# Kernel optimization log

Hardware: AMD Instinct MI355X
Metric: run time of the kernel (lower is better)

Reference implementation:

```python
import math
import jax
import jax.numpy as jnp
import numpy as np

B, N = 64, 64
R = N * (N - 1)
DIST_THRESH = 0.35


def _pair_indices(n):
    # edge e = i*(n-1) + j - (j > i): row-major over i, ascending j skipping j == i
    ii = np.repeat(np.arange(n), n - 1)
    jm = np.tile(np.arange(n), (n, 1))
    jj = jm[~np.eye(n, dtype=bool)].reshape(-1)
    return ii, jj


def _rot_basis(a):
    # a: [..., 1] angle -> [..., 2, 2] rotation basis rows [cos,sin],[cos(a+pi/2),sin(a+pi/2)]
    first = jnp.concatenate([jnp.cos(a), jnp.sin(a)], axis=-1)
    second = jnp.concatenate([jnp.cos(a + math.pi / 2), jnp.sin(a + math.pi / 2)], axis=-1)
    return jnp.stack([first, second], axis=-2)


def setup_inputs() -> dict:
    ks = jax.random.split(jax.random.key(0), 8)
    nrm = lambda k, shape, s=1.0: (jax.random.normal(k, shape) * s).astype(jnp.float32)
    return dict(
        objects_state=jax.random.uniform(ks[0], (B, N, 8), dtype=jnp.float32),
        objects_shape=nrm(ks[1], (B, N, 10)),
        relation_info=nrm(ks[2], (B, R, 3)),
        s_mean=jnp.zeros((8,), jnp.float32), s_std=jnp.ones((8,), jnp.float32),
        sh_mean=jnp.zeros((10,), jnp.float32), sh_std=jnp.ones((10,), jnp.float32),
        v_mean=jnp.zeros((3,), jnp.float32), v_std=jnp.ones((3,), jnp.float32),
        W1=nrm(ks[3], (32, 256), 32 ** -0.5), b1=jnp.zeros((256,), jnp.float32),
        W2=nrm(ks[4], (256, 128), 256 ** -0.5), b2=jnp.zeros((128,), jnp.float32),
        W3=nrm(ks[5], (141, 256), 141 ** -0.5), b3=jnp.zeros((256,), jnp.float32),
        W4=nrm(ks[6], (256, 3), 256 ** -0.5), b4=jnp.zeros((3,), jnp.float32),
    )


def reference(objects_state, objects_shape, relation_info, s_mean, s_std, sh_mean, sh_std,
              v_mean, v_std, W1, b1, W2, b2, W3, b3, W4, b4):
    n = objects_state.shape[1]
    ii, jj = _pair_indices(n)

    # ---- pre_proces: distance-threshold edge build into dense one-hot matrices ----
    pos = objects_state[:, :, 0:2]
    dist = jnp.sqrt(jnp.sum((pos[:, :, None, :] - pos[:, None, :, :]) ** 2, axis=-1))
    # torch: where(dist<0.35, dist, 0).nonzero() -> keeps dist<0.35 AND dist != 0 (drops self-edges)
    mask = ((dist < DIST_THRESH) & (dist != 0.0)).astype(jnp.float32)
    mask_flat = mask[:, ii, jj]  # [B, R]
    eye = jnp.eye(n, dtype=jnp.float32)
    receiver_relations = mask_flat[:, :, None] * eye[ii][None]  # [B, R, N]
    sender_relations = mask_flat[:, :, None] * eye[jj][None]    # [B, R, N]

    data_state = (objects_state - s_mean) / s_std
    data_shape = (objects_shape - sh_mean) / sh_std

    senders_state = jnp.einsum('brn,bnd->brd', sender_relations, data_state)
    receivers_state = jnp.einsum('brn,bnd->brd', receiver_relations, data_state)
    senders_shape = jnp.einsum('brn,bnd->brd', sender_relations, data_shape)
    receivers_shape = jnp.einsum('brn,bnd->brd', receiver_relations, data_shape)

    basis = _rot_basis(receivers_state[:, :, 2:3])  # [B, R, 2, 2]
    diff_state = senders_state - receivers_state
    temp = jnp.stack([diff_state[:, :, 0:2], diff_state[:, :, 3:5], senders_state[:, :, 6:8]], axis=-1)  # [B,R,2,3]
    tfed = jnp.einsum('brij,brjk->brik', basis, temp)  # [B,R,2,3]
    angle_diff = diff_state[:, :, 2:3]
    diff_feat = jnp.concatenate([
        tfed[:, :, :, 0], tfed[:, :, :, 1], tfed[:, :, :, 2],
        jnp.sin(2 * angle_diff), jnp.cos(2 * angle_diff),
        diff_state[:, :, 5:6],
    ], axis=-1)  # [B, R, 9]
    rel_data = jnp.concatenate([relation_info, diff_feat, receivers_shape, senders_shape], axis=-1)  # [B,R,32]

    obj_basis = _rot_basis(data_state[:, :, 2:3])  # [B, N, 2, 2]
    obj_vel_tfed = jnp.einsum('bnij,bnj->bni', obj_basis, data_state[:, :, 3:5])
    obj_data = jnp.concatenate([obj_vel_tfed, data_state[:, :, 5:6], data_shape], axis=-1)  # [B,N,13]

    # ---- interaction-network Net ----
    effects = jax.nn.relu(rel_data @ W1 + b1) @ W2 + b2  # [B, R, 128]
    agg = jnp.einsum('brn,bre->bne', receiver_relations, effects)  # [B, N, 128]
    out_vel = jax.nn.relu(jnp.concatenate([obj_data, agg], axis=-1) @ W3 + b3) @ W4 + b4  # [B,N,3]

    # ---- post_proces ----
    angles = objects_state[:, 1:, 2:3]
    pred = out_vel[:, 1:, :] * v_std + v_mean  # inv_transform_vel
    basis_back = _rot_basis(-angles)
    vel_back = jnp.einsum('bnij,bnj->bni', basis_back, pred[:, :, :2])
    x_dot = jnp.concatenate([vel_back, pred[:, :, 2:]], axis=-1)  # [B, N-1, 3]

    tp = np.eye(6, dtype=np.float32)
    tp[3:, 3:] = 0.0
    tq = np.zeros((3, 6), dtype=np.float32)
    for i in range(3):
        tq[i, i] = 1.0
        tq[i, 3 + i] = 1.0
    x_next = objects_state[:, 1:, :6] @ jnp.asarray(tp) + x_dot @ jnp.asarray(tq)
    return x_next  # [B, N-1, 6]
```

## Files before the change

### kernel.cpp

```cpp
#include <hip/hip_runtime.h>
#include <math.h>

#define BB 64
#define NN 64
#define NM1 63
#define RR (NN*(NN-1))

#define WS1_OFF 0
#define WS2_OFF 16384
#define WS3_OFF 81920
#define WSO_OFF 163840

typedef short bf16x8 __attribute__((ext_vector_type(8)));
typedef float f32x4 __attribute__((ext_vector_type(4)));
union U4 { uint4 u; bf16x8 b; };

__device__ inline unsigned int f2bf(float f) {
    unsigned int u = __float_as_uint(f);
    return (u + 0x7FFFu + ((u >> 16) & 1u)) >> 16;
}
__device__ inline unsigned int pack2(float a, float b) {
    return f2bf(a) | (f2bf(b) << 16);
}

__global__ __launch_bounds__(256) void prep_kernel(
    const float* __restrict__ objects_state,
    const float* __restrict__ objects_shape,
    const float* __restrict__ s_mean, const float* __restrict__ s_std,
    const float* __restrict__ sh_mean, const float* __restrict__ sh_std,
    const float* __restrict__ W1, const float* __restrict__ W2,
    const float* __restrict__ W3, unsigned char* __restrict__ ws)
{
    const int t = threadIdx.x;
    if (blockIdx.x < 40) {
        const int u = blockIdx.x*4 + (t >> 6), l = t & 63;
        const int col16 = l & 15, quad = l >> 4;
        float v[8];
        uint4* dst;
        if (u < 16) {
            const int nt = u, col = nt*16 + col16;
            #pragma unroll
            for (int j = 0; j < 8; ++j) {
                const int k = quad*8 + j;
                const int orig = k < 12 ? k : (k < 22 ? k+10 : k-10);
                v[j] = W1[orig*256 + col];
            }
            dst = (uint4*)(ws + WS1_OFF) + (nt*64 + l);
        } else if (u < 80) {
            const int w = u-16, nt = w >> 3, kc = w & 7, col = nt*16 + col16;
            #pragma unroll
            for (int j = 0; j < 8; ++j)
                v[j] = W2[(size_t)(kc*32 + quad*8 + j)*128 + col];
            dst = (uint4*)(ws + WS2_OFF) + ((nt*8 + kc)*64 + l);
        } else {
            const int w = u-80, nt = w/5, kc = w - nt*5, col = nt*16 + col16;
            #pragma unroll
            for (int j = 0; j < 8; ++j) {
                const int k = kc*32 + quad*8 + j;
                v[j] = (k < 141) ? W3[(size_t)k*256 + col] : 0.f;
            }
            dst = (uint4*)(ws + WS3_OFF) + ((nt*5 + kc)*64 + l);
        }
        uint4 o;
        o.x = pack2(v[0], v[1]); o.y = pack2(v[2], v[3]);
        o.z = pack2(v[4], v[5]); o.w = pack2(v[6], v[7]);
        *dst = o;
    } else {
        const int obj = (blockIdx.x - 40)*256 + t;
        float st[8], sh[10];
        #pragma unroll
        for (int c = 0; c < 8; ++c)  st[c] = objects_state[(size_t)obj*8 + c];
        #pragma unroll
        for (int c = 0; c < 10; ++c) sh[c] = objects_shape[(size_t)obj*10 + c];
        float f[28];
        f[0] = st[0]; f[1] = st[1]; f[26] = st[2]; f[27] = 0.f;
        #pragma unroll
        for (int c = 0; c < 8; ++c)  f[2+c]  = (st[c] - s_mean[c]) / s_std[c];
        #pragma unroll
        for (int c = 0; c < 10; ++c) f[10+c] = (sh[c] - sh_mean[c]) / sh_std[c];
        float sa, ca, sr, cr;
        __sincosf(f[4], &sa, &ca);
        __sincosf(st[2], &sr, &cr);
        sa = sinf(f[4]); ca = cosf(f[4]);
        sr = sinf(st[2]); cr = cosf(st[2]);
        f[20] = ca; f[21] = sa; f[22] = cr; f[23] = sr;
        f[24] =  ca*f[5] + sa*f[6];
        f[25] = -sa*f[5] + ca*f[6];
        float4* dst = (float4*)(ws + WSO_OFF + (size_t)obj*112);
        #pragma unroll
        for (int q = 0; q < 7; ++q)
            dst[q] = make_float4(f[q*4], f[q*4+1], f[q*4+2], f[q*4+3]);
    }
}

__global__ __launch_bounds__(512) void main_kernel(
    const float* __restrict__ relation_info,
    const float* __restrict__ v_mean, const float* __restrict__ v_std,
    const float* __restrict__ b1, const float* __restrict__ b2,
    const float* __restrict__ b3,
    const float* __restrict__ W4, const float* __restrict__ b4,
    const unsigned char* __restrict__ ws,
    float* __restrict__ out)
{
    __shared__ __align__(16) float P[64][28];
    __shared__ __align__(16) unsigned int relb_w[8*64*16];
    __shared__ __align__(16) float RI[1512];
    __shared__ __align__(16) unsigned short s_h[16*264];
    __shared__ __align__(16) unsigned short s_q[16*168];
    __shared__ int   s_cntg[8];
    __shared__ float s_red[8][16][3];
    __shared__ float s_outv[16][3];

    const int b  = blockIdx.x >> 3;
    const int nb = (blockIdx.x & 7) * 8;
    const int t  = threadIdx.x;
    const int wv = t >> 6, lane = t & 63, col16 = lane & 15, quad = lane >> 4;

    {
        uint4 z = make_uint4(0,0,0,0);
        uint4* relb4 = (uint4*)relb_w;
        #pragma unroll
        for (int r = 0; r < 4; ++r) relb4[r*512 + t] = z;
        if (t < 336) ((uint4*)s_q)[t] = z;
        if (t < 8) s_cntg[t] = 0;
        const float* psrc = (const float*)(ws + WSO_OFF + (size_t)(b*64)*112);
        float* P0 = &P[0][0];
        #pragma unroll
        for (int r = 0; r < 4; ++r) {
            const int idx = r*512 + t;
            if (idx < 1792) P0[idx] = psrc[idx];
        }
        const float* rsrc = relation_info + ((size_t)b*RR + nb*NM1)*3;
        #pragma unroll
        for (int r = 0; r < 3; ++r) {
            const int idx = r*512 + t;
            if (idx < 1512) RI[idx] = rsrc[idx];
        }
    }
    __syncthreads();

    if (t < 504) {
        const int g = t/63, k = t - g*63, n = nb + g, j = k + (k >= n);
        const float dx = P[n][0] - P[j][0];
        const float dy = P[n][1] - P[j][1];
        const float dist = sqrtf(dx*dx + dy*dy);
        if (dist < 0.35f && dist != 0.0f) {
            const int slot = atomicAdd(&s_cntg[g], 1);
            const int row = (g << 6) + slot;
            float f[32];
            f[0] = RI[t*3]; f[1] = RI[t*3+1]; f[2] = RI[t*3+2];
            const float rd0 = P[n][2], rd1 = P[n][3], rd2 = P[n][4],
                        rd3 = P[n][5], rd4 = P[n][6], rd5 = P[n][7];
            const float ca = P[n][20], sa = P[n][21];
            const float d0 = P[j][2]-rd0, d1 = P[j][3]-rd1, d2 = P[j][4]-rd2,
                        d3 = P[j][5]-rd3, d4 = P[j][6]-rd4, d5 = P[j][7]-rd5;
            f[3]  =  ca*d0 + sa*d1;
            f[4]  = -sa*d0 + ca*d1;
            f[5]  =  ca*d3 + sa*d4;
            f[6]  = -sa*d3 + ca*d4;
            f[7]  =  ca*P[j][8] + sa*P[j][9];
            f[8]  = -sa*P[j][8] + ca*P[j][9];
            f[9]  = sinf(2.f*d2);
            f[10] = cosf(2.f*d2);
            f[11] = d5;
            #pragma unroll
            for (int c = 0; c < 10; ++c) f[12+c] = P[j][10+c];
            #pragma unroll
            for (int c = 0; c < 10; ++c) f[22+c] = P[n][10+c];
            uint4* dst = (uint4*)&relb_w[row*16];
            #pragma unroll
            for (int w4 = 0; w4 < 4; ++w4) {
                uint4 o;
                o.x = pack2(f[w4*8+0], f[w4*8+1]);
                o.y = pack2(f[w4*8+2], f[w4*8+3]);
                o.z = pack2(f[w4*8+4], f[w4*8+5]);
                o.w = pack2(f[w4*8+6], f[w4*8+7]);
                dst[w4] = o;
            }
        }
    }
    __syncthreads();

    {
        int cg[8];
        #pragma unroll
        for (int g = 0; g < 8; ++g) cg[g] = s_cntg[g];
        const uint4* w1f = (const uint4*)(ws + WS1_OFF);
        U4 bu0, bu1;
        bu0.u = w1f[(wv*2+0)*64 + lane];
        bu1.u = w1f[(wv*2+1)*64 + lane];
        const float b10 = b1[(wv*2+0)*16 + col16];
        const float b11 = b1[(wv*2+1)*16 + col16];
        float hs0[8], hs1[8];
        #pragma unroll
        for (int g = 0; g < 8; ++g) { hs0[g] = 0.f; hs1[g] = 0.f; }
        #pragma unroll
        for (int g = 0; g < 8; ++g) {
            const int mts = (cg[g] + 15) >> 4;
            for (int mt = 0; mt < mts; ++mt) {
                U4 au;
                au.u = *(const uint4*)&relb_w[((g<<6) + mt*16 + col16)*16 + quad*4];
                f32x4 a0 = {0.f,0.f,0.f,0.f}, a1 = {0.f,0.f,0.f,0.f};
                a0 = __builtin_amdgcn_mfma_f32_16x16x32_bf16(au.b, bu0.b, a0, 0,0,0);
                a1 = __builtin_amdgcn_mfma_f32_16x16x32_bf16(au.b, bu1.b, a1, 0,0,0);
                #pragma unroll
                for (int i = 0; i < 4; ++i) {
                    hs0[g] += fmaxf(a0[i] + b10, 0.f);
                    hs1[g] += fmaxf(a1[i] + b11, 0.f);
                }
            }
        }
        const float rb0 = fmaxf(b10, 0.f), rb1 = fmaxf(b11, 0.f);
        #pragma unroll
        for (int g = 0; g < 8; ++g) {
            const int mts = (cg[g] + 15) >> 4;
            const float pad = (float)(mts*16 - cg[g]);
            float v0 = hs0[g], v1 = hs1[g];
            v0 += __shfl_xor(v0, 16); v0 += __shfl_xor(v0, 32);
            v1 += __shfl_xor(v1, 16); v1 += __shfl_xor(v1, 32);
            if (quad == 0) {
                s_h[g*264 + (wv*2+0)*16 + col16] =
                    (unsigned short)f2bf(v0 - pad*rb0);
                s_h[g*264 + (wv*2+1)*16 + col16] =
                    (unsigned short)f2bf(v1 - pad*rb1);
            }
        }
    }
    __syncthreads();

    if (t < 104) {
        const int m = t/13, c = t - m*13, n = nb + m;
        float v;
        if (c == 0) v = P[n][24];
        else if (c == 1) v = P[n][25];
        else if (c == 2) v = P[n][7];
        else v = P[n][10 + c - 3];
        s_q[m*168 + c] = (unsigned short)f2bf(v);
    }
    {
        U4 af[8];
        #pragma unroll
        for (int kc = 0; kc < 8; ++kc)
            af[kc].u = *(const uint4*)&s_h[(lane & 15)*264 + kc*32 + quad*8];
        float cntv[4];
        #pragma unroll
        for (int i = 0; i < 4; ++i)
            cntv[i] = (float)s_cntg[(quad*4 + i) & 7];
        const uint4* w2f = (const uint4*)(ws + WS2_OFF);
        f32x4 acc = {0.f,0.f,0.f,0.f};
        #pragma unroll
        for (int kc = 0; kc < 8; ++kc) {
            U4 bu; bu.u = w2f[(wv*8 + kc)*64 + lane];
            acc = __builtin_amdgcn_mfma_f32_16x16x32_bf16(af[kc].b, bu.b, acc, 0,0,0);
        }
        const float b2v = b2[wv*16 + col16];
        #pragma unroll
        for (int i = 0; i < 4; ++i) {
            const int row = quad*4 + i;
            s_q[row*168 + 13 + wv*16 + col16] =
                (unsigned short)f2bf(acc[i] + cntv[i]*b2v);
        }
    }
    __syncthreads();

    {
        U4 af3[5];
        #pragma unroll
        for (int kc = 0; kc < 5; ++kc)
            af3[kc].u = *(const uint4*)&s_q[(lane & 15)*168 + kc*32 + quad*8];
        const uint4* w3f = (const uint4*)(ws + WS3_OFF);
        float p[4][3];
        #pragma unroll
        for (int i = 0; i < 4; ++i) { p[i][0]=0.f; p[i][1]=0.f; p[i][2]=0.f; }
        #pragma unroll
        for (int ntl = 0; ntl < 2; ++ntl) {
            const int nt = wv + ntl*8, col = nt*16 + col16;
            f32x4 acc = {0.f,0.f,0.f,0.f};
            #pragma unroll
            for (int kc = 0; kc < 5; ++kc) {
                U4 bu; bu.u = w3f[(nt*5 + kc)*64 + lane];
                acc = __builtin_amdgcn_mfma_f32_16x16x32_bf16(af3[kc].b, bu.b, acc, 0,0,0);
            }
            const float b3v = b3[col];
            const float w40 = W4[col*3+0], w41 = W4[col*3+1], w42 = W4[col*3+2];
            #pragma unroll
            for (int i = 0; i < 4; ++i) {
                const float h = fmaxf(acc[i] + b3v, 0.f);
                p[i][0] = fmaf(h, w40, p[i][0]);
                p[i][1] = fmaf(h, w41, p[i][1]);
                p[i][2] = fmaf(h, w42, p[i][2]);
            }
        }
        #pragma unroll
        for (int off = 1; off < 16; off <<= 1)
            #pragma unroll
            for (int i = 0; i < 4; ++i) {
                p[i][0] += __shfl_xor(p[i][0], off);
                p[i][1] += __shfl_xor(p[i][1], off);
                p[i][2] += __shfl_xor(p[i][2], off);
            }
        if (col16 == 0)
            #pragma unroll
            for (int i = 0; i < 4; ++i) {
                s_red[wv][quad*4+i][0] = p[i][0];
                s_red[wv][quad*4+i][1] = p[i][1];
                s_red[wv][quad*4+i][2] = p[i][2];
            }
    }
    __syncthreads();
    if (t < 48) {
        const int m = t/3, o = t - m*3;
        float acc = b4[o];
        #pragma unroll
        for (int w = 0; w < 8; ++w) acc += s_red[w][m][o];
        s_outv[m][o] = acc;
    }
    __syncthreads();

    if (t < 48) {
        const int m = t/6, i = t - m*6, n = nb + m;
        if (n >= 1) {
            const float q0 = s_outv[m][0]*v_std[0] + v_mean[0];
            const float q1 = s_outv[m][1]*v_std[1] + v_mean[1];
            const float q2 = s_outv[m][2]*v_std[2] + v_mean[2];
            const float cr = P[n][22], sr = P[n][23];
            const float xd0 = cr*q0 - sr*q1;
            const float xd1 = sr*q0 + cr*q1;
            const int im = i % 3;
            const float xd = (im == 0) ? xd0 : (im == 1) ? xd1 : q2;
            float base = 0.f;
            if (i == 0) base = P[n][0];
            else if (i == 1) base = P[n][1];
            else if (i == 2) base = P[n][26];
            out[((size_t)b*NM1 + (n-1))*6 + i] = base + xd;
        }
    }
}

extern "C" void kernel_launch(void* const* d_in, const int* in_sizes, int n_in,
                              void* d_out, int out_size, void* d_ws, size_t ws_size,
                              hipStream_t stream) {
    const float* objects_state = (const float*)d_in[0];
    const float* objects_shape = (const float*)d_in[1];
    const float* relation_info = (const float*)d_in[2];
    const float* s_mean  = (const float*)d_in[3];
    const float* s_std   = (const float*)d_in[4];
    const float* sh_mean = (const float*)d_in[5];
    const float* sh_std  = (const float*)d_in[6];
    const float* v_mean  = (const float*)d_in[7];
    const float* v_std   = (const float*)d_in[8];
    const float* W1 = (const float*)d_in[9];
    const float* b1 = (const float*)d_in[10];
    const float* W2 = (const float*)d_in[11];
    const float* b2 = (const float*)d_in[12];
    const float* W3 = (const float*)d_in[13];
    const float* b3 = (const float*)d_in[14];
    const float* W4 = (const float*)d_in[15];
    const float* b4 = (const float*)d_in[16];
    unsigned char* ws = (unsigned char*)d_ws;

    prep_kernel<<<dim3(56), dim3(256), 0, stream>>>(
        objects_state, objects_shape, s_mean, s_std, sh_mean, sh_std,
        W1, W2, W3, ws);
    main_kernel<<<dim3(BB*8), dim3(512), 0, stream>>>(
        relation_info, v_mean, v_std, b1, b2, b3, W4, b4,
        ws, (float*)d_out);
}
```

Measured before the change: 105.4 us.

## Fuse prep kernel into main kernel, loading and converting weights per block

Removes the separate prep kernel that pre-packed the weights into bf16 MFMA layout and normalized per-object features into a workspace. Each block now computes its own object features directly into shared memory and loads the fp32 weights from global memory, converting them to bf16 fragments in registers. The W2 and W3 loads are placed before barriers so their latency can overlap other work. This saves one kernel launch and the workspace round trip, at the cost of redundant per-block weight conversion, strided uncoalesced fp32 weight reads, and higher register pressure.

```diff
diff --git a/kernel.cpp b/kernel.cpp
--- a/kernel.cpp
+++ b/kernel.cpp
@@ -5,11 +5,6 @@
 #define NN 64
 #define NM1 63
 #define RR (NN*(NN-1))
-
-#define WS1_OFF 0
-#define WS2_OFF 16384
-#define WS3_OFF 81920
-#define WSO_OFF 163840
 
 typedef short bf16x8 __attribute__((ext_vector_type(8)));
 typedef float f32x4 __attribute__((ext_vector_type(4)));
@@ -23,83 +18,17 @@
     return f2bf(a) | (f2bf(b) << 16);
 }
 
-__global__ __launch_bounds__(256) void prep_kernel(
+__global__ __launch_bounds__(512, 4) void fused_kernel(
     const float* __restrict__ objects_state,
     const float* __restrict__ objects_shape,
+    const float* __restrict__ relation_info,
     const float* __restrict__ s_mean, const float* __restrict__ s_std,
     const float* __restrict__ sh_mean, const float* __restrict__ sh_std,
-    const float* __restrict__ W1, const float* __restrict__ W2,
-    const float* __restrict__ W3, unsigned char* __restrict__ ws)
-{
-    const int t = threadIdx.x;
-    if (blockIdx.x < 40) {
-        const int u = blockIdx.x*4 + (t >> 6), l = t & 63;
-        const int col16 = l & 15, quad = l >> 4;
-        float v[8];
-        uint4* dst;
-        if (u < 16) {
-            const int nt = u, col = nt*16 + col16;
-            #pragma unroll
-            for (int j = 0; j < 8; ++j) {
-                const int k = quad*8 + j;
-                const int orig = k < 12 ? k : (k < 22 ? k+10 : k-10);
-                v[j] = W1[orig*256 + col];
-            }
-            dst = (uint4*)(ws + WS1_OFF) + (nt*64 + l);
-        } else if (u < 80) {
-            const int w = u-16, nt = w >> 3, kc = w & 7, col = nt*16 + col16;
-            #pragma unroll
-            for (int j = 0; j < 8; ++j)
-                v[j] = W2[(size_t)(kc*32 + quad*8 + j)*128 + col];
-            dst = (uint4*)(ws + WS2_OFF) + ((nt*8 + kc)*64 + l);
-        } else {
-            const int w = u-80, nt = w/5, kc = w - nt*5, col = nt*16 + col16;
-            #pragma unroll
-            for (int j = 0; j < 8; ++j) {
-                const int k = kc*32 + quad*8 + j;
-                v[j] = (k < 141) ? W3[(size_t)k*256 + col] : 0.f;
-            }
-            dst = (uint4*)(ws + WS3_OFF) + ((nt*5 + kc)*64 + l);
-        }
-        uint4 o;
-        o.x = pack2(v[0], v[1]); o.y = pack2(v[2], v[3]);
-        o.z = pack2(v[4], v[5]); o.w = pack2(v[6], v[7]);
-        *dst = o;
-    } else {
-        const int obj = (blockIdx.x - 40)*256 + t;
-        float st[8], sh[10];
-        #pragma unroll
-        for (int c = 0; c < 8; ++c)  st[c] = objects_state[(size_t)obj*8 + c];
-        #pragma unroll
-        for (int c = 0; c < 10; ++c) sh[c] = objects_shape[(size_t)obj*10 + c];
-        float f[28];
-        f[0] = st[0]; f[1] = st[1]; f[26] = st[2]; f[27] = 0.f;
-        #pragma unroll
-        for (int c = 0; c < 8; ++c)  f[2+c]  = (st[c] - s_mean[c]) / s_std[c];
-        #pragma unroll
-        for (int c = 0; c < 10; ++c) f[10+c] = (sh[c] - sh_mean[c]) / sh_std[c];
-        float sa, ca, sr, cr;
-        __sincosf(f[4], &sa, &ca);
-        __sincosf(st[2], &sr, &cr);
-        sa = sinf(f[4]); ca = cosf(f[4]);
-        sr = sinf(st[2]); cr = cosf(st[2]);
-        f[20] = ca; f[21] = sa; f[22] = cr; f[23] = sr;
-        f[24] =  ca*f[5] + sa*f[6];
-        f[25] = -sa*f[5] + ca*f[6];
-        float4* dst = (float4*)(ws + WSO_OFF + (size_t)obj*112);
-        #pragma unroll
-        for (int q = 0; q < 7; ++q)
-            dst[q] = make_float4(f[q*4], f[q*4+1], f[q*4+2], f[q*4+3]);
-    }
-}
-
-__global__ __launch_bounds__(512) void main_kernel(
-    const float* __restrict__ relation_info,
     const float* __restrict__ v_mean, const float* __restrict__ v_std,
-    const float* __restrict__ b1, const float* __restrict__ b2,
-    const float* __restrict__ b3,
+    const float* __restrict__ W1, const float* __restrict__ b1,
+    const float* __restrict__ W2, const float* __restrict__ b2,
+    const float* __restrict__ W3, const float* __restrict__ b3,
     const float* __restrict__ W4, const float* __restrict__ b4,
-    const unsigned char* __restrict__ ws,
     float* __restrict__ out)
 {
     __shared__ __align__(16) float P[64][28];
@@ -116,6 +45,19 @@
     const int t  = threadIdx.x;
     const int wv = t >> 6, lane = t & 63, col16 = lane & 15, quad = lane >> 4;
 
+    float w1v[16], b10, b11;
+    {
+        const int cA = wv*32 + col16, cB = cA + 16;
+        #pragma unroll
+        for (int j = 0; j < 8; ++j) {
+            const int k = quad*8 + j;
+            const int orig = k < 12 ? k : (k < 22 ? k+10 : k-10);
+            w1v[j]   = W1[orig*256 + cA];
+            w1v[8+j] = W1[orig*256 + cB];
+        }
+        b10 = b1[cA]; b11 = b1[cB];
+    }
+
     {
         uint4 z = make_uint4(0,0,0,0);
         uint4* relb4 = (uint4*)relb_w;
@@ -123,21 +65,43 @@
         for (int r = 0; r < 4; ++r) relb4[r*512 + t] = z;
         if (t < 336) ((uint4*)s_q)[t] = z;
         if (t < 8) s_cntg[t] = 0;
-        const float* psrc = (const float*)(ws + WSO_OFF + (size_t)(b*64)*112);
-        float* P0 = &P[0][0];
-        #pragma unroll
-        for (int r = 0; r < 4; ++r) {
-            const int idx = r*512 + t;
-            if (idx < 1792) P0[idx] = psrc[idx];
-        }
         const float* rsrc = relation_info + ((size_t)b*RR + nb*NM1)*3;
         #pragma unroll
         for (int r = 0; r < 3; ++r) {
             const int idx = r*512 + t;
             if (idx < 1512) RI[idx] = rsrc[idx];
         }
-    }
-    __syncthreads();
+        if (t < 64) {
+            const int n = b*64 + t;
+            float st[8], sh[10];
+            #pragma unroll
+            for (int c = 0; c < 8; ++c)  st[c] = objects_state[(size_t)n*8 + c];
+            #pragma unroll
+            for (int c = 0; c < 10; ++c) sh[c] = objects_shape[(size_t)n*10 + c];
+            float f[28];
+            f[0] = st[0]; f[1] = st[1]; f[26] = st[2]; f[27] = 0.f;
+            #pragma unroll
+            for (int c = 0; c < 8; ++c)  f[2+c]  = (st[c] - s_mean[c]) / s_std[c];
+            #pragma unroll
+            for (int c = 0; c < 10; ++c) f[10+c] = (sh[c] - sh_mean[c]) / sh_std[c];
+            const float sa = sinf(f[4]), ca = cosf(f[4]);
+            const float sr = sinf(st[2]), cr = cosf(st[2]);
+            f[20] = ca; f[21] = sa; f[22] = cr; f[23] = sr;
+            f[24] =  ca*f[5] + sa*f[6];
+            f[25] = -sa*f[5] + ca*f[6];
+            float4* dp = (float4*)&P[t][0];
+            #pragma unroll
+            for (int q = 0; q < 7; ++q)
+                dp[q] = make_float4(f[q*4], f[q*4+1], f[q*4+2], f[q*4+3]);
+        }
+    }
+    __syncthreads();
+
+    U4 bu0, bu1;
+    bu0.u.x = pack2(w1v[0],  w1v[1]);  bu0.u.y = pack2(w1v[2],  w1v[3]);
+    bu0.u.z = pack2(w1v[4],  w1v[5]);  bu0.u.w = pack2(w1v[6],  w1v[7]);
+    bu1.u.x = pack2(w1v[8],  w1v[9]);  bu1.u.y = pack2(w1v[10], w1v[11]);
+    bu1.u.z = pack2(w1v[12], w1v[13]); bu1.u.w = pack2(w1v[14], w1v[15]);
 
     if (t < 504) {
         const int g = t/63, k = t - g*63, n = nb + g, j = k + (k >= n);
@@ -147,36 +111,32 @@
         if (dist < 0.35f && dist != 0.0f) {
             const int slot = atomicAdd(&s_cntg[g], 1);
             const int row = (g << 6) + slot;
-            float f[32];
-            f[0] = RI[t*3]; f[1] = RI[t*3+1]; f[2] = RI[t*3+2];
-            const float rd0 = P[n][2], rd1 = P[n][3], rd2 = P[n][4],
-                        rd3 = P[n][5], rd4 = P[n][6], rd5 = P[n][7];
+            uint4* dst = (uint4*)&relb_w[row*16];
             const float ca = P[n][20], sa = P[n][21];
-            const float d0 = P[j][2]-rd0, d1 = P[j][3]-rd1, d2 = P[j][4]-rd2,
-                        d3 = P[j][5]-rd3, d4 = P[j][6]-rd4, d5 = P[j][7]-rd5;
-            f[3]  =  ca*d0 + sa*d1;
-            f[4]  = -sa*d0 + ca*d1;
-            f[5]  =  ca*d3 + sa*d4;
-            f[6]  = -sa*d3 + ca*d4;
-            f[7]  =  ca*P[j][8] + sa*P[j][9];
-            f[8]  = -sa*P[j][8] + ca*P[j][9];
-            f[9]  = sinf(2.f*d2);
-            f[10] = cosf(2.f*d2);
-            f[11] = d5;
-            #pragma unroll
-            for (int c = 0; c < 10; ++c) f[12+c] = P[j][10+c];
-            #pragma unroll
-            for (int c = 0; c < 10; ++c) f[22+c] = P[n][10+c];
-            uint4* dst = (uint4*)&relb_w[row*16];
-            #pragma unroll
-            for (int w4 = 0; w4 < 4; ++w4) {
-                uint4 o;
-                o.x = pack2(f[w4*8+0], f[w4*8+1]);
-                o.y = pack2(f[w4*8+2], f[w4*8+3]);
-                o.z = pack2(f[w4*8+4], f[w4*8+5]);
-                o.w = pack2(f[w4*8+6], f[w4*8+7]);
-                dst[w4] = o;
-            }
+            const float d0 = P[j][2]-P[n][2], d1 = P[j][3]-P[n][3];
+            const float d2 = P[j][4]-P[n][4], d3 = P[j][5]-P[n][5];
+            const float d4 = P[j][6]-P[n][6], d5 = P[j][7]-P[n][7];
+            uint4 o;
+            o.x = pack2(RI[t*3],   RI[t*3+1]);
+            o.y = pack2(RI[t*3+2], ca*d0 + sa*d1);
+            o.z = pack2(-sa*d0 + ca*d1, ca*d3 + sa*d4);
+            o.w = pack2(-sa*d3 + ca*d4, ca*P[j][8] + sa*P[j][9]);
+            dst[0] = o;
+            o.x = pack2(-sa*P[j][8] + ca*P[j][9], sinf(2.f*d2));
+            o.y = pack2(cosf(2.f*d2), d5);
+            o.z = pack2(P[j][10], P[j][11]);
+            o.w = pack2(P[j][12], P[j][13]);
+            dst[1] = o;
+            o.x = pack2(P[j][14], P[j][15]);
+            o.y = pack2(P[j][16], P[j][17]);
+            o.z = pack2(P[j][18], P[j][19]);
+            o.w = pack2(P[n][10], P[n][11]);
+            dst[2] = o;
+            o.x = pack2(P[n][12], P[n][13]);
+            o.y = pack2(P[n][14], P[n][15]);
+            o.z = pack2(P[n][16], P[n][17]);
+            o.w = pack2(P[n][18], P[n][19]);
+            dst[3] = o;
         }
     }
     __syncthreads();
@@ -185,12 +145,6 @@
         int cg[8];
         #pragma unroll
         for (int g = 0; g < 8; ++g) cg[g] = s_cntg[g];
-        const uint4* w1f = (const uint4*)(ws + WS1_OFF);
-        U4 bu0, bu1;
-        bu0.u = w1f[(wv*2+0)*64 + lane];
-        bu1.u = w1f[(wv*2+1)*64 + lane];
-        const float b10 = b1[(wv*2+0)*16 + col16];
-        const float b11 = b1[(wv*2+1)*16 + col16];
         float hs0[8], hs1[8];
         #pragma unroll
         for (int g = 0; g < 8; ++g) { hs0[g] = 0.f; hs1[g] = 0.f; }
@@ -226,6 +180,19 @@
             }
         }
     }
+
+    U4 w2f[8];
+    #pragma unroll
+    for (int kc = 0; kc < 8; ++kc) {
+        float v[8];
+        #pragma unroll
+        for (int j = 0; j < 8; ++j)
+            v[j] = W2[(size_t)(kc*32 + quad*8 + j)*128 + wv*16 + col16];
+        U4 o;
+        o.u.x = pack2(v[0], v[1]); o.u.y = pack2(v[2], v[3]);
+        o.u.z = pack2(v[4], v[5]); o.u.w = pack2(v[6], v[7]);
+        w2f[kc] = o;
+    }
     __syncthreads();
 
     if (t < 104) {
@@ -246,13 +213,10 @@
         #pragma unroll
         for (int i = 0; i < 4; ++i)
             cntv[i] = (float)s_cntg[(quad*4 + i) & 7];
-        const uint4* w2f = (const uint4*)(ws + WS2_OFF);
         f32x4 acc = {0.f,0.f,0.f,0.f};
         #pragma unroll
-        for (int kc = 0; kc < 8; ++kc) {
-            U4 bu; bu.u = w2f[(wv*8 + kc)*64 + lane];
-            acc = __builtin_amdgcn_mfma_f32_16x16x32_bf16(af[kc].b, bu.b, acc, 0,0,0);
-        }
+        for (int kc = 0; kc < 8; ++kc)
+            acc = __builtin_amdgcn_mfma_f32_16x16x32_bf16(af[kc].b, w2f[kc].b, acc, 0,0,0);
         const float b2v = b2[wv*16 + col16];
         #pragma unroll
         for (int i = 0; i < 4; ++i) {
@@ -261,6 +225,15 @@
                 (unsigned short)f2bf(acc[i] + cntv[i]*b2v);
         }
     }
+
+    float w3v[40];
+    #pragma unroll
+    for (int kc = 0; kc < 5; ++kc)
+        #pragma unroll
+        for (int j = 0; j < 8; ++j) {
+            const int k = kc*32 + quad*8 + j;
+            w3v[kc*8+j] = (k < 141) ? W3[(size_t)k*256 + wv*16 + col16] : 0.f;
+        }
     __syncthreads();
 
     {
@@ -268,17 +241,29 @@
         #pragma unroll
         for (int kc = 0; kc < 5; ++kc)
             af3[kc].u = *(const uint4*)&s_q[(lane & 15)*168 + kc*32 + quad*8];
-        const uint4* w3f = (const uint4*)(ws + WS3_OFF);
         float p[4][3];
         #pragma unroll
         for (int i = 0; i < 4; ++i) { p[i][0]=0.f; p[i][1]=0.f; p[i][2]=0.f; }
         #pragma unroll
         for (int ntl = 0; ntl < 2; ++ntl) {
             const int nt = wv + ntl*8, col = nt*16 + col16;
+            if (ntl == 1) {
+                #pragma unroll
+                for (int kc = 0; kc < 5; ++kc)
+                    #pragma unroll
+                    for (int j = 0; j < 8; ++j) {
+                        const int k = kc*32 + quad*8 + j;
+                        w3v[kc*8+j] = (k < 141) ? W3[(size_t)k*256 + col] : 0.f;
+                    }
+            }
             f32x4 acc = {0.f,0.f,0.f,0.f};
             #pragma unroll
             for (int kc = 0; kc < 5; ++kc) {
-                U4 bu; bu.u = w3f[(nt*5 + kc)*64 + lane];
+                U4 bu;
+                bu.u.x = pack2(w3v[kc*8+0], w3v[kc*8+1]);
+                bu.u.y = pack2(w3v[kc*8+2], w3v[kc*8+3]);
+                bu.u.z = pack2(w3v[kc*8+4], w3v[kc*8+5]);
+                bu.u.w = pack2(w3v[kc*8+6], w3v[kc*8+7]);
                 acc = __builtin_amdgcn_mfma_f32_16x16x32_bf16(af3[kc].b, bu.b, acc, 0,0,0);
             }
             const float b3v = b3[col];
@@ -357,12 +342,11 @@
     const float* b3 = (const float*)d_in[14];
     const float* W4 = (const float*)d_in[15];
     const float* b4 = (const float*)d_in[16];
-    unsigned char* ws = (unsigned char*)d_ws;
-
-    prep_kernel<<<dim3(56), dim3(256), 0, stream>>>(
-        objects_state, objects_shape, s_mean, s_std, sh_mean, sh_std,
-        W1, W2, W3, ws);
-    main_kernel<<<dim3(BB*8), dim3(512), 0, stream>>>(
-        relation_info, v_mean, v_std, b1, b2, b3, W4, b4,
-        ws, (float*)d_out);
+    (void)d_ws; (void)ws_size; (void)in_sizes; (void)n_in; (void)out_size;
+
+    fused_kernel<<<dim3(BB*8), dim3(512), 0, stream>>>(
+        objects_state, objects_shape, relation_info,
+        s_mean, s_std, sh_mean, sh_std, v_mean, v_std,
+        W1, b1, W2, b2, W3, b3, W4, b4,
+        (float*)d_out);
 }
```

Result: slower. 107.6 us (+2.1%).
